# Performance work log

Measured on AMD Instinct MI355X. Metric: run time of the kernel, lower is better.

The kernel has to match this reference:

```python
import jax, jax.numpy as jnp
import numpy as np
from jax import lax

NUM_VARS = 16384
NUM_CHECKS = 8192
BATCH = 32
MAX_ITER = 15
H_DENSITY = 0.001  # ~8 ones per column, LDPC-like Tanner graph


def setup_inputs() -> dict:
    key = jax.random.key(0)
    k_h, k_s, k_l = jax.random.split(key, 3)
    # Sparse binary parity-check matrix represented densely (same math).
    parity_matrix = (jax.random.uniform(k_h, (NUM_CHECKS, NUM_VARS)) < H_DENSITY).astype(jnp.float32)
    syndrome = jax.random.randint(k_s, (BATCH, NUM_CHECKS), 0, 2).astype(jnp.float32)
    channel_llrs = jax.random.normal(k_l, (BATCH, NUM_VARS), dtype=jnp.float32)
    w_vc = jnp.ones((1,), dtype=jnp.float32)
    w_cv = jnp.ones((1,), dtype=jnp.float32)
    damping = jnp.float32(0.5)
    return {
        "syndrome": syndrome,
        "parity_matrix": parity_matrix,
        "channel_llrs": channel_llrs,
        "w_vc": w_vc,
        "w_cv": w_cv,
        "damping": damping,
    }


def reference(syndrome, parity_matrix, channel_llrs, w_vc, w_cv, damping):
    # syndrome: (B, C); parity_matrix H: (C, V); channel_llrs: (B, V)
    s_sign = 1.0 - 2.0 * syndrome  # (B, C)

    def body(v_beliefs, _):
        # v -> c: sparse.mm(H, v^T)^T == v @ H^T  -> (B, C)
        v_to_c = w_vc * (v_beliefs @ parity_matrix.T)
        c_msg = s_sign * jnp.tanh(v_to_c * 0.5)  # (B, C)
        # c -> v: sparse.mm(H^T, c^T)^T == c @ H  -> (B, V)
        c_to_v = w_cv * (c_msg @ parity_matrix)
        v_new = damping * v_beliefs + (1.0 - damping) * (channel_llrs + c_to_v)
        return v_new, None

    v_beliefs, _ = lax.scan(body, channel_llrs, None, length=MAX_ITER)
    return jax.nn.sigmoid(-v_beliefs)  # (B, V) bit-flip probabilities
```

## Files before the change

### kernel.cpp

```cpp
#include <hip/hip_runtime.h>


#define C_NUM 8192
#define V_NUM 16384
#define B_NUM 32
#define RW 64
#define CW 32

#define RQ 12
#define CQ 8

#define NBLK 256
#define NTHR 1024
#define NTH (NBLK * NTHR)

#define WCAP 256

typedef unsigned short u16;
typedef unsigned int u32;
typedef unsigned long long u64;

#define ZERO_WORDS ((C_NUM * 4 + V_NUM * 4 + C_NUM * RW * 2 + V_NUM * CW * 2) / 4)
#define NBAR 31
#define BAR_STRIDE 64

__device__ __forceinline__ float agent_ldf(const float* p) {
    return __hip_atomic_load(p, __ATOMIC_RELAXED, __HIP_MEMORY_SCOPE_AGENT);
}
__device__ __forceinline__ void agent_stf(float* p, float v) {
    __hip_atomic_store(p, v, __ATOMIC_RELAXED, __HIP_MEMORY_SCOPE_AGENT);
}
__device__ __forceinline__ u64 agent_ld64(const u64* p) {
    return __hip_atomic_load(p, __ATOMIC_RELAXED, __HIP_MEMORY_SCOPE_AGENT);
}
__device__ __forceinline__ int agent_ldi(const int* p) {
    return __hip_atomic_load(p, __ATOMIC_RELAXED, __HIP_MEMORY_SCOPE_AGENT);
}
__device__ __forceinline__ void agent_st32(u32* p, u32 v) {
    __hip_atomic_store(p, v, __ATOMIC_RELAXED, __HIP_MEMORY_SCOPE_AGENT);
}
__device__ __forceinline__ void agent_st16(u16* p, u16 v) {
    __hip_atomic_store(p, v, __ATOMIC_RELAXED, __HIP_MEMORY_SCOPE_AGENT);
}

__device__ __forceinline__ void grid_barrier(u32* bars, int id) {
    __syncthreads();
    if (threadIdx.x == 0) {
        u32* base = bars + id * 8 * BAR_STRIDE;
        asm volatile("s_waitcnt vmcnt(0) lgkmcnt(0)" ::: "memory");
        __hip_atomic_fetch_add(base + (blockIdx.x & 7) * BAR_STRIDE, 1u,
                               __ATOMIC_RELAXED, __HIP_MEMORY_SCOPE_AGENT);
        u32 sum;
        do {
            sum = 0;
#pragma unroll
            for (int g = 0; g < 8; ++g)
                sum += __hip_atomic_load(base + g * BAR_STRIDE,
                                         __ATOMIC_RELAXED, __HIP_MEMORY_SCOPE_AGENT);
            if (sum < (u32)NBLK) __builtin_amdgcn_s_sleep(4);
        } while (sum < (u32)NBLK);
        asm volatile("" ::: "memory");
    }
    __syncthreads();
}

__device__ __forceinline__ float fast_tanh_half(float x) {
    float ax = fabsf(x);
    float e = __expf(-ax);
    return copysignf((1.0f - e) / (1.0f + e), x);
}

__global__ __launch_bounds__(NTHR, 1)
void bp_fused(const float* __restrict__ H,
              const float* __restrict__ synd,
              const float* __restrict__ llr,
              const float* __restrict__ w_vc_p,
              const float* __restrict__ w_cv_p,
              const float* __restrict__ damp_p,
              int* __restrict__ row_cnt, int* __restrict__ col_cnt,
              u16* __restrict__ row_idx, u16* __restrict__ col_idx,
              float* __restrict__ bel, float* __restrict__ cms,
              u32* __restrict__ bars,
              float* __restrict__ out) {
    const int tid = blockIdx.x * NTHR + threadIdx.x;
    const int lane = threadIdx.x & 63;

    __shared__ u32 lds_edges[(NTHR / 64) * WCAP];
    __shared__ u64 ls_row64[32 * RQ];
    __shared__ u64 ls_col64[64 * CQ];
    u32* const wl = lds_edges + (threadIdx.x >> 6) * WCAP;

    {
        u32* zp = (u32*)row_cnt;
        for (int t = tid; t < ZERO_WORDS; t += NTH) agent_st32(&zp[t], 0u);
        if (tid < 32) agent_stf(&bel[V_NUM * B_NUM + tid], 0.0f);
        else if (tid < 64) agent_stf(&cms[C_NUM * B_NUM + (tid - 32)], 0.0f);
    }
    float llr_r[2], bel_r[2];
#pragma unroll
    for (int r = 0; r < 2; ++r) {
        int i = tid + r * NTH;
        int b = i & 31, v = i >> 5;
        float x = llr[b * V_NUM + v];
        llr_r[r] = x; bel_r[r] = x;
        agent_stf(&bel[i], x);
    }
    float ss_r;
    {
        int b = tid & 31, c = tid >> 5;
        ss_r = 1.0f - 2.0f * synd[b * C_NUM + c];
    }

    int wave_cnt;
    {
        const float4* Hv = (const float4*)H;
        const u64 ltmask = (1ull << lane) - 1ull;
        int wb = 0;
        int t = tid;
        float4 c0 = Hv[t];
        float4 c1 = Hv[t + NTH];
#pragma unroll 1
        for (int itn = 0; itn < 64; ++itn) {
            float4 n0, n1;
            int tn = t + 2 * NTH;
            if (itn < 63) { n0 = Hv[tn]; n1 = Hv[tn + NTH]; }
            float vals[8] = {c0.x, c0.y, c0.z, c0.w, c1.x, c1.y, c1.z, c1.w};
#pragma unroll
            for (int k = 0; k < 8; ++k) {
                bool nz = vals[k] != 0.0f;
                u64 b = __ballot(nz);
                if (b) {
                    if (nz) {
                        int ee = (k < 4) ? (t * 4 + k)
                                         : ((t + NTH) * 4 + (k - 4));
                        int off = wb + (int)__popcll(b & ltmask);
                        if (off < WCAP) wl[off] = (u32)ee;
                    }
                    wb += (int)__popcll(b);
                }
            }
            c0 = n0; c1 = n1; t = tn;
        }
        wave_cnt = wb < WCAP ? wb : WCAP;
    }
    grid_barrier(bars, 0);

    {
        for (int e = lane; e < wave_cnt; e += 64) {
            u32 ee = wl[e];
            int c = (int)(ee >> 14);
            int v = (int)(ee & (V_NUM - 1));
            int rs = atomicAdd(&row_cnt[c], 1);
            if (rs < RW) agent_st16(&row_idx[c * RW + rs], (u16)v);
            int cs = atomicAdd(&col_cnt[v], 1);
            if (cs < CW) agent_st16(&col_idx[v * CW + cs], (u16)c);
        }
    }
    grid_barrier(bars, 1);

    {
        int t = threadIdx.x;
        if (t < 32 * RQ) {
            int g = t / RQ, p = t - g * RQ;
            int c = (blockIdx.x << 5) + g;
            int n = agent_ldi(&row_cnt[c]);
            n = n > 4 * RQ ? 4 * RQ : n;
            u64 q = agent_ld64(&((const u64*)(row_idx + c * RW))[p]);
            int j = 4 * p;
            u64 a0 = (j + 0 < n) ? (q & 0xFFFFu) : (u64)V_NUM;
            u64 a1 = (j + 1 < n) ? ((q >> 16) & 0xFFFFu) : (u64)V_NUM;
            u64 a2 = (j + 2 < n) ? ((q >> 32) & 0xFFFFu) : (u64)V_NUM;
            u64 a3 = (j + 3 < n) ? (q >> 48) : (u64)V_NUM;
            ls_row64[t] = a0 | (a1 << 16) | (a2 << 32) | (a3 << 48);
        } else if (t >= 512) {
            int t2 = t - 512;
            int g = t2 >> 3, p = t2 & 7;
            int v = (g < 32) ? ((blockIdx.x << 5) + g)
                             : (C_NUM + (blockIdx.x << 5) + (g - 32));
            int n = agent_ldi(&col_cnt[v]);
            n = n > 4 * CQ ? 4 * CQ : n;
            u64 q = agent_ld64(&((const u64*)(col_idx + v * CW))[p]);
            int j = 4 * p;
            u64 a0 = (j + 0 < n) ? (q & 0xFFFFu) : (u64)C_NUM;
            u64 a1 = (j + 1 < n) ? ((q >> 16) & 0xFFFFu) : (u64)C_NUM;
            u64 a2 = (j + 2 < n) ? ((q >> 32) & 0xFFFFu) : (u64)C_NUM;
            u64 a3 = (j + 3 < n) ? (q >> 48) : (u64)C_NUM;
            ls_col64[t2] = a0 | (a1 << 16) | (a2 << 32) | (a3 << 48);
        }
    }
    int nrow_r;
    {
        int n = agent_ldi(&row_cnt[tid >> 5]);
        nrow_r = n > 4 * RQ ? 4 * RQ : n;
    }
    int ncol_r[2];
#pragma unroll
    for (int r = 0; r < 2; ++r) {
        int n = agent_ldi(&col_cnt[(tid + r * NTH) >> 5]);
        ncol_r[r] = n > 4 * CQ ? 4 * CQ : n;
    }
    const float wvc = w_vc_p[0];
    const float wcv = w_cv_p[0];
    const float d   = damp_p[0];
    __syncthreads();

    const int b_lo = tid & 31;
    const u64* const rowL  = ls_row64 + (threadIdx.x >> 5) * RQ;
    const u64* const colL0 = ls_col64 + (threadIdx.x >> 5) * CQ;
    const u64* const colL1 = ls_col64 + (32 + (threadIdx.x >> 5)) * CQ;
    int barid = 2;
    for (int it = 0; it < 15; ++it) {
        {
            float sum = 0.0f;
#pragma unroll
            for (int p = 0; p < RQ; ++p) {
                if (4 * p < nrow_r) {
                    u64 q = rowL[p];
                    int i0 = (int)(q & 0xFFFFu);
                    int i1 = (int)((q >> 16) & 0xFFFFu);
                    int i2 = (int)((q >> 32) & 0xFFFFu);
                    int i3 = (int)(q >> 48);
                    float s0 = agent_ldf(&bel[i0 * B_NUM + b_lo]);
                    float s1 = agent_ldf(&bel[i1 * B_NUM + b_lo]);
                    float s2 = agent_ldf(&bel[i2 * B_NUM + b_lo]);
                    float s3 = agent_ldf(&bel[i3 * B_NUM + b_lo]);
                    sum += s0; sum += s1; sum += s2; sum += s3;
                }
            }
            agent_stf(&cms[tid], ss_r * fast_tanh_half(wvc * sum));
        }
        grid_barrier(bars, barid++);

        bool last = (it == 14);
#pragma unroll
        for (int r = 0; r < 2; ++r) {
            const u64* colL = r ? colL1 : colL0;
            float sum = 0.0f;
#pragma unroll
            for (int p = 0; p < CQ; ++p) {
                if (4 * p < ncol_r[r]) {
                    u64 q = colL[p];
                    int i0 = (int)(q & 0xFFFFu);
                    int i1 = (int)((q >> 16) & 0xFFFFu);
                    int i2 = (int)((q >> 32) & 0xFFFFu);
                    int i3 = (int)(q >> 48);
                    float s0 = agent_ldf(&cms[i0 * B_NUM + b_lo]);
                    float s1 = agent_ldf(&cms[i1 * B_NUM + b_lo]);
                    float s2 = agent_ldf(&cms[i2 * B_NUM + b_lo]);
                    float s3 = agent_ldf(&cms[i3 * B_NUM + b_lo]);
                    sum += s0; sum += s1; sum += s2; sum += s3;
                }
            }
            float nb = d * bel_r[r] + (1.0f - d) * (llr_r[r] + wcv * sum);
            bel_r[r] = nb;
            int i = tid + r * NTH;
            if (!last) {
                agent_stf(&bel[i], nb);
            } else {
                int b = i & 31, v = i >> 5;
                out[b * V_NUM + v] = 1.0f / (1.0f + __expf(nb));
            }
        }
        if (!last) grid_barrier(bars, barid++);
    }
}

extern "C" void kernel_launch(void* const* d_in, const int* in_sizes, int n_in,
                              void* d_out, int out_size, void* d_ws, size_t ws_size,
                              hipStream_t stream) {
    const float* synd = (const float*)d_in[0];
    const float* H    = (const float*)d_in[1];
    const float* llr  = (const float*)d_in[2];
    const float* w_vc = (const float*)d_in[3];
    const float* w_cv = (const float*)d_in[4];
    const float* damp = (const float*)d_in[5];
    float* out = (float*)d_out;

    char* ws = (char*)d_ws;
    size_t off = 0;
    int* row_cnt = (int*)(ws + off); off += (size_t)C_NUM * 4;
    int* col_cnt = (int*)(ws + off); off += (size_t)V_NUM * 4;
    u16* row_idx = (u16*)(ws + off); off += (size_t)C_NUM * RW * 2;
    u16* col_idx = (u16*)(ws + off); off += (size_t)V_NUM * CW * 2;
    float* bel = (float*)(ws + off); off += (size_t)V_NUM * B_NUM * 4 + 256;
    float* cms = (float*)(ws + off); off += (size_t)C_NUM * B_NUM * 4 + 256;
    u32* bars  = (u32*)(ws + off); off += (size_t)NBAR * 8 * BAR_STRIDE * 4;

    hipMemsetAsync(bars, 0, (size_t)NBAR * 8 * BAR_STRIDE * 4, stream);

    void* args[] = {
        (void*)&H, (void*)&synd, (void*)&llr,
        (void*)&w_vc, (void*)&w_cv, (void*)&damp,
        (void*)&row_cnt, (void*)&col_cnt, (void*)&row_idx, (void*)&col_idx,
        (void*)&bel, (void*)&cms, (void*)&bars, (void*)&out
    };
    hipLaunchCooperativeKernel((const void*)bp_fused,
                               dim3(NBLK), dim3(NTHR), args, 0, stream);
}
```

Measured before the change: 927.3 us.

## Replace check-to-variable grid barrier with per-value epoch-tagged flags

Check messages are now stored as 64-bit words that pack the float with an iteration tag. They go into double-buffered arrays, and variable nodes spin on each needed message until its tag matches the current iteration. This removes one grid-wide barrier per iteration so variable updates can start as soon as their inputs are ready. The H scan prefetch is also deepened to two stages ahead. In exchange, message traffic doubles in width, extra zeroing is needed, and polling loops may add memory contention.

```diff
diff --git a/kernel.cpp b/kernel.cpp
--- a/kernel.cpp
+++ b/kernel.cpp
@@ -20,7 +20,9 @@
 typedef unsigned int u32;
 typedef unsigned long long u64;
 
-#define ZERO_WORDS ((C_NUM * 4 + V_NUM * 4 + C_NUM * RW * 2 + V_NUM * CW * 2) / 4)
+#define CSTRIDE (C_NUM * B_NUM + 32)
+#define ZW_A ((C_NUM * 4 + V_NUM * 4 + C_NUM * RW * 2 + V_NUM * CW * 2 + C_NUM * B_NUM * 8) / 4)
+#define ZW_B (C_NUM * B_NUM * 8 / 4)
 #define NBAR 31
 #define BAR_STRIDE 64
 
@@ -32,6 +34,9 @@
 }
 __device__ __forceinline__ u64 agent_ld64(const u64* p) {
     return __hip_atomic_load(p, __ATOMIC_RELAXED, __HIP_MEMORY_SCOPE_AGENT);
+}
+__device__ __forceinline__ void agent_st64(u64* p, u64 v) {
+    __hip_atomic_store(p, v, __ATOMIC_RELAXED, __HIP_MEMORY_SCOPE_AGENT);
 }
 __device__ __forceinline__ int agent_ldi(const int* p) {
     return __hip_atomic_load(p, __ATOMIC_RELAXED, __HIP_MEMORY_SCOPE_AGENT);
@@ -79,7 +84,8 @@
               const float* __restrict__ damp_p,
               int* __restrict__ row_cnt, int* __restrict__ col_cnt,
               u16* __restrict__ row_idx, u16* __restrict__ col_idx,
-              float* __restrict__ bel, float* __restrict__ cms,
+              u64* __restrict__ cmst,
+              float* __restrict__ bel,
               u32* __restrict__ bars,
               float* __restrict__ out) {
     const int tid = blockIdx.x * NTHR + threadIdx.x;
@@ -92,9 +98,14 @@
 
     {
         u32* zp = (u32*)row_cnt;
-        for (int t = tid; t < ZERO_WORDS; t += NTH) agent_st32(&zp[t], 0u);
+        for (int t = tid; t < ZW_A; t += NTH) agent_st32(&zp[t], 0u);
+        u32* zq = (u32*)(cmst + CSTRIDE);
+        for (int t = tid; t < ZW_B; t += NTH) agent_st32(&zq[t], 0u);
         if (tid < 32) agent_stf(&bel[V_NUM * B_NUM + tid], 0.0f);
-        else if (tid < 64) agent_stf(&cms[C_NUM * B_NUM + (tid - 32)], 0.0f);
+        else if (tid < 64)
+            agent_st64(&cmst[C_NUM * B_NUM + (tid - 32)], 0xFFFFFFFF00000000ull);
+        else if (tid < 96)
+            agent_st64(&cmst[CSTRIDE + C_NUM * B_NUM + (tid - 64)], 0xFFFFFFFF00000000ull);
     }
     float llr_r[2], bel_r[2];
 #pragma unroll
@@ -116,30 +127,31 @@
         const float4* Hv = (const float4*)H;
         const u64 ltmask = (1ull << lane) - 1ull;
         int wb = 0;
-        int t = tid;
-        float4 c0 = Hv[t];
-        float4 c1 = Hv[t + NTH];
+        int ta = tid;
+        int tb = tid + 2 * NTH;
+        float4 a0 = Hv[ta], a1 = Hv[ta + NTH];
+        float4 b0 = Hv[tb], b1 = Hv[tb + NTH];
 #pragma unroll 1
         for (int itn = 0; itn < 64; ++itn) {
-            float4 n0, n1;
-            int tn = t + 2 * NTH;
-            if (itn < 63) { n0 = Hv[tn]; n1 = Hv[tn + NTH]; }
-            float vals[8] = {c0.x, c0.y, c0.z, c0.w, c1.x, c1.y, c1.z, c1.w};
+            int tc = tb + 2 * NTH;
+            float4 p0, p1;
+            if (itn < 62) { p0 = Hv[tc]; p1 = Hv[tc + NTH]; }
+            float vals[8] = {a0.x, a0.y, a0.z, a0.w, a1.x, a1.y, a1.z, a1.w};
 #pragma unroll
             for (int k = 0; k < 8; ++k) {
                 bool nz = vals[k] != 0.0f;
                 u64 b = __ballot(nz);
                 if (b) {
                     if (nz) {
-                        int ee = (k < 4) ? (t * 4 + k)
-                                         : ((t + NTH) * 4 + (k - 4));
+                        int ee = (k < 4) ? (ta * 4 + k)
+                                         : ((ta + NTH) * 4 + (k - 4));
                         int off = wb + (int)__popcll(b & ltmask);
                         if (off < WCAP) wl[off] = (u32)ee;
                     }
                     wb += (int)__popcll(b);
                 }
             }
-            c0 = n0; c1 = n1; t = tn;
+            a0 = b0; a1 = b1; b0 = p0; b1 = p1; ta = tb; tb = tc;
         }
         wave_cnt = wb < WCAP ? wb : WCAP;
     }
@@ -210,6 +222,8 @@
     const u64* const colL1 = ls_col64 + (32 + (threadIdx.x >> 5)) * CQ;
     int barid = 2;
     for (int it = 0; it < 15; ++it) {
+        const u32 want = (u32)(it + 1);
+        u64* const cw = cmst + (size_t)(it & 1) * CSTRIDE;
         {
             float sum = 0.0f;
 #pragma unroll
@@ -227,9 +241,9 @@
                     sum += s0; sum += s1; sum += s2; sum += s3;
                 }
             }
-            agent_stf(&cms[tid], ss_r * fast_tanh_half(wvc * sum));
-        }
-        grid_barrier(bars, barid++);
+            float m = ss_r * fast_tanh_half(wvc * sum);
+            agent_st64(&cw[tid], ((u64)want << 32) | (u64)__float_as_uint(m));
+        }
 
         bool last = (it == 14);
 #pragma unroll
@@ -244,11 +258,30 @@
                     int i1 = (int)((q >> 16) & 0xFFFFu);
                     int i2 = (int)((q >> 32) & 0xFFFFu);
                     int i3 = (int)(q >> 48);
-                    float s0 = agent_ldf(&cms[i0 * B_NUM + b_lo]);
-                    float s1 = agent_ldf(&cms[i1 * B_NUM + b_lo]);
-                    float s2 = agent_ldf(&cms[i2 * B_NUM + b_lo]);
-                    float s3 = agent_ldf(&cms[i3 * B_NUM + b_lo]);
-                    sum += s0; sum += s1; sum += s2; sum += s3;
+                    u64* a0 = &cw[(size_t)i0 * B_NUM + b_lo];
+                    u64* a1 = &cw[(size_t)i1 * B_NUM + b_lo];
+                    u64* a2 = &cw[(size_t)i2 * B_NUM + b_lo];
+                    u64* a3 = &cw[(size_t)i3 * B_NUM + b_lo];
+                    u64 g0 = agent_ld64(a0);
+                    u64 g1 = agent_ld64(a1);
+                    u64 g2 = agent_ld64(a2);
+                    u64 g3 = agent_ld64(a3);
+                    for (;;) {
+                        bool bad0 = (u32)(g0 >> 32) < want;
+                        bool bad1 = (u32)(g1 >> 32) < want;
+                        bool bad2 = (u32)(g2 >> 32) < want;
+                        bool bad3 = (u32)(g3 >> 32) < want;
+                        if (!(bad0 | bad1 | bad2 | bad3)) break;
+                        __builtin_amdgcn_s_sleep(1);
+                        if (bad0) g0 = agent_ld64(a0);
+                        if (bad1) g1 = agent_ld64(a1);
+                        if (bad2) g2 = agent_ld64(a2);
+                        if (bad3) g3 = agent_ld64(a3);
+                    }
+                    sum += __uint_as_float((u32)g0);
+                    sum += __uint_as_float((u32)g1);
+                    sum += __uint_as_float((u32)g2);
+                    sum += __uint_as_float((u32)g3);
                 }
             }
             float nb = d * bel_r[r] + (1.0f - d) * (llr_r[r] + wcv * sum);
@@ -282,8 +315,8 @@
     int* col_cnt = (int*)(ws + off); off += (size_t)V_NUM * 4;
     u16* row_idx = (u16*)(ws + off); off += (size_t)C_NUM * RW * 2;
     u16* col_idx = (u16*)(ws + off); off += (size_t)V_NUM * CW * 2;
-    float* bel = (float*)(ws + off); off += (size_t)V_NUM * B_NUM * 4 + 256;
-    float* cms = (float*)(ws + off); off += (size_t)C_NUM * B_NUM * 4 + 256;
+    u64* cmst = (u64*)(ws + off); off += (size_t)2 * CSTRIDE * 8;
+    float* bel = (float*)(ws + off); off += (size_t)(V_NUM * B_NUM + 64) * 4;
     u32* bars  = (u32*)(ws + off); off += (size_t)NBAR * 8 * BAR_STRIDE * 4;
 
     hipMemsetAsync(bars, 0, (size_t)NBAR * 8 * BAR_STRIDE * 4, stream);
@@ -292,7 +325,7 @@
         (void*)&H, (void*)&synd, (void*)&llr,
         (void*)&w_vc, (void*)&w_cv, (void*)&damp,
         (void*)&row_cnt, (void*)&col_cnt, (void*)&row_idx, (void*)&col_idx,
-        (void*)&bel, (void*)&cms, (void*)&bars, (void*)&out
+        (void*)&cmst, (void*)&bel, (void*)&bars, (void*)&out
     };
     hipLaunchCooperativeKernel((const void*)bp_fused,
                                dim3(NBLK), dim3(NTHR), args, 0, stream);
```

Measured after the change: 925.5 us. Within noise of the previous version (-0.2%).

## Partition batch across XCDs so BP iterations use XCD-local L2 loads

Applied to the files above, without the earlier changes.

Each block reads its XCC_ID from a hardware register and takes a rank within that XCD. When all 8 XCDs hold 32 blocks each, every XCD owns 4 batch columns and stores them in its own belief and check-message slice. The iteration gathers then use sc0 loads (cached in the XCD's L2) rather than agent-scope coherent loads, which is meant to cut cross-die coherence traffic. In exchange it needs a bigger LDS footprint, drops the zeroing of row_idx and col_idx, and deepens the prefetch in the H scan. If the XCD mapping is unbalanced it falls back to agent-scope loads.

```diff
diff --git a/kernel.cpp b/kernel.cpp
--- a/kernel.cpp
+++ b/kernel.cpp
@@ -9,6 +9,8 @@
 
 #define RQ 12
 #define CQ 8
+#define RQ_S 13
+#define CQ_S 9
 
 #define NBLK 256
 #define NTHR 1024
@@ -16,12 +18,15 @@
 
 #define WCAP 256
 
+#define BEL_SL (16400 * 4)
+#define CMS_SL (8200 * 4)
+
 typedef unsigned short u16;
 typedef unsigned int u32;
 typedef unsigned long long u64;
 
-#define ZERO_WORDS ((C_NUM * 4 + V_NUM * 4 + C_NUM * RW * 2 + V_NUM * CW * 2) / 4)
-#define NBAR 31
+#define ZERO_WORDS ((C_NUM + V_NUM))
+#define NBAR 32
 #define BAR_STRIDE 64
 
 __device__ __forceinline__ float agent_ldf(const float* p) {
@@ -70,6 +75,159 @@
     return copysignf((1.0f - e) / (1.0f + e), x);
 }
 
+template<bool LOCAL>
+__device__ __forceinline__ void ld4(const float* p0, const float* p1,
+                                    const float* p2, const float* p3,
+                                    float& r0, float& r1, float& r2, float& r3) {
+    if (LOCAL) {
+        asm volatile(
+            "global_load_dword %0, %4, off sc0\n\t"
+            "global_load_dword %1, %5, off sc0\n\t"
+            "global_load_dword %2, %6, off sc0\n\t"
+            "global_load_dword %3, %7, off sc0\n\t"
+            "s_waitcnt vmcnt(0)"
+            : "=&v"(r0), "=&v"(r1), "=&v"(r2), "=&v"(r3)
+            : "v"(p0), "v"(p1), "v"(p2), "v"(p3)
+            : "memory");
+    } else {
+        r0 = agent_ldf(p0); r1 = agent_ldf(p1);
+        r2 = agent_ldf(p2); r3 = agent_ldf(p3);
+    }
+}
+
+template<bool LOCAL>
+__device__ __forceinline__ void decode_tail(
+    int G, int R,
+    const float* __restrict__ synd, const float* __restrict__ llr,
+    const int* __restrict__ row_cnt, const int* __restrict__ col_cnt,
+    const u16* __restrict__ row_idx, const u16* __restrict__ col_idx,
+    float* __restrict__ bel_x, float* __restrict__ cms_x,
+    u32* __restrict__ bars, float* __restrict__ out,
+    u64* ls_row, u64* ls_col,
+    float wvc, float wcv, float d)
+{
+    const int t = threadIdx.x;
+    const int b4 = t & 3;
+    const int qid = t >> 2;
+    float* const belS = bel_x + (size_t)G * BEL_SL;
+    float* const cmsS = cms_x + (size_t)G * CMS_SL;
+
+    for (int e = t; e < 256 * RQ; e += NTHR) {
+        int rl = e / RQ, p = e - rl * RQ;
+        int c = (R << 8) + rl;
+        int n = agent_ldi(&row_cnt[c]); n = n > 4 * RQ ? 4 * RQ : n;
+        u64 q = agent_ld64(&((const u64*)(row_idx + (size_t)c * RW))[p]);
+        int j = 4 * p;
+        u64 a0 = (j + 0 < n) ? (q & 0xFFFFu) : (u64)V_NUM;
+        u64 a1 = (j + 1 < n) ? ((q >> 16) & 0xFFFFu) : (u64)V_NUM;
+        u64 a2 = (j + 2 < n) ? ((q >> 32) & 0xFFFFu) : (u64)V_NUM;
+        u64 a3 = (j + 3 < n) ? (q >> 48) : (u64)V_NUM;
+        ls_row[rl * RQ_S + p] = a0 | (a1 << 16) | (a2 << 32) | (a3 << 48);
+    }
+    for (int e = t; e < 512 * CQ; e += NTHR) {
+        int gl = e >> 3, p = e & 7;
+        int v = (gl < 256) ? ((R << 8) + gl) : (C_NUM + (R << 8) + (gl - 256));
+        int n = agent_ldi(&col_cnt[v]); n = n > 4 * CQ ? 4 * CQ : n;
+        u64 q = agent_ld64(&((const u64*)(col_idx + (size_t)v * CW))[p]);
+        int j = 4 * p;
+        u64 a0 = (j + 0 < n) ? (q & 0xFFFFu) : (u64)C_NUM;
+        u64 a1 = (j + 1 < n) ? ((q >> 16) & 0xFFFFu) : (u64)C_NUM;
+        u64 a2 = (j + 2 < n) ? ((q >> 32) & 0xFFFFu) : (u64)C_NUM;
+        u64 a3 = (j + 3 < n) ? (q >> 48) : (u64)C_NUM;
+        ls_col[gl * CQ_S + p] = a0 | (a1 << 16) | (a2 << 32) | (a3 << 48);
+    }
+    const int c_my = (R << 8) + qid;
+    const int v0_my = (R << 8) + qid;
+    const int v1_my = C_NUM + (R << 8) + qid;
+    int nrow;  { int n = agent_ldi(&row_cnt[c_my]);  nrow  = n > 4*RQ ? 4*RQ : n; }
+    int ncol0; { int n = agent_ldi(&col_cnt[v0_my]); ncol0 = n > 4*CQ ? 4*CQ : n; }
+    int ncol1; { int n = agent_ldi(&col_cnt[v1_my]); ncol1 = n > 4*CQ ? 4*CQ : n; }
+    const int b = (G << 2) + b4;
+    const float ss = 1.0f - 2.0f * synd[b * C_NUM + c_my];
+    const float llr0 = llr[b * V_NUM + v0_my];
+    const float llr1 = llr[b * V_NUM + v1_my];
+    float bel0 = llr0, bel1 = llr1;
+    if (LOCAL) {
+        belS[v0_my * 4 + b4] = bel0;
+        belS[v1_my * 4 + b4] = bel1;
+    } else {
+        agent_stf(&belS[v0_my * 4 + b4], bel0);
+        agent_stf(&belS[v1_my * 4 + b4], bel1);
+    }
+
+    grid_barrier(bars, 2);
+
+    const u64* const rowL  = ls_row + qid * RQ_S;
+    const u64* const colL0 = ls_col + qid * CQ_S;
+    const u64* const colL1 = ls_col + (256 + qid) * CQ_S;
+    float* const cms_own  = cmsS + c_my * 4 + b4;
+    float* const bel_own0 = belS + v0_my * 4 + b4;
+    float* const bel_own1 = belS + v1_my * 4 + b4;
+
+    int barid = 3;
+    for (int it = 0; it < 15; ++it) {
+        {
+            float sum = 0.0f;
+#pragma unroll
+            for (int p = 0; p < RQ; ++p) {
+                if (4 * p < nrow) {
+                    u64 q = rowL[p];
+                    const float* a0 = belS + (int)(q & 0xFFFFu) * 4 + b4;
+                    const float* a1 = belS + (int)((q >> 16) & 0xFFFFu) * 4 + b4;
+                    const float* a2 = belS + (int)((q >> 32) & 0xFFFFu) * 4 + b4;
+                    const float* a3 = belS + (int)(q >> 48) * 4 + b4;
+                    float s0, s1, s2, s3;
+                    ld4<LOCAL>(a0, a1, a2, a3, s0, s1, s2, s3);
+                    sum += s0; sum += s1; sum += s2; sum += s3;
+                }
+            }
+            float m = ss * fast_tanh_half(wvc * sum);
+            if (LOCAL) *cms_own = m; else agent_stf(cms_own, m);
+        }
+        grid_barrier(bars, barid++);
+
+        bool last = (it == 14);
+        float sum0 = 0.0f, sum1 = 0.0f;
+#pragma unroll
+        for (int p = 0; p < CQ; ++p) {
+            if (4 * p < ncol0) {
+                u64 q = colL0[p];
+                const float* a0 = cmsS + (int)(q & 0xFFFFu) * 4 + b4;
+                const float* a1 = cmsS + (int)((q >> 16) & 0xFFFFu) * 4 + b4;
+                const float* a2 = cmsS + (int)((q >> 32) & 0xFFFFu) * 4 + b4;
+                const float* a3 = cmsS + (int)(q >> 48) * 4 + b4;
+                float s0, s1, s2, s3;
+                ld4<LOCAL>(a0, a1, a2, a3, s0, s1, s2, s3);
+                sum0 += s0; sum0 += s1; sum0 += s2; sum0 += s3;
+            }
+        }
+#pragma unroll
+        for (int p = 0; p < CQ; ++p) {
+            if (4 * p < ncol1) {
+                u64 q = colL1[p];
+                const float* a0 = cmsS + (int)(q & 0xFFFFu) * 4 + b4;
+                const float* a1 = cmsS + (int)((q >> 16) & 0xFFFFu) * 4 + b4;
+                const float* a2 = cmsS + (int)((q >> 32) & 0xFFFFu) * 4 + b4;
+                const float* a3 = cmsS + (int)(q >> 48) * 4 + b4;
+                float s0, s1, s2, s3;
+                ld4<LOCAL>(a0, a1, a2, a3, s0, s1, s2, s3);
+                sum1 += s0; sum1 += s1; sum1 += s2; sum1 += s3;
+            }
+        }
+        float nb0 = d * bel0 + (1.0f - d) * (llr0 + wcv * sum0);
+        float nb1 = d * bel1 + (1.0f - d) * (llr1 + wcv * sum1);
+        bel0 = nb0; bel1 = nb1;
+        if (!last) {
+            if (LOCAL) { *bel_own0 = nb0; *bel_own1 = nb1; }
+            else { agent_stf(bel_own0, nb0); agent_stf(bel_own1, nb1); }
+            grid_barrier(bars, barid++);
+        } else {
+            out[b * V_NUM + v0_my] = 1.0f / (1.0f + __expf(nb0));
+            out[b * V_NUM + v1_my] = 1.0f / (1.0f + __expf(nb1));
+        }
+    }
+}
+
 __global__ __launch_bounds__(NTHR, 1)
 void bp_fused(const float* __restrict__ H,
               const float* __restrict__ synd,
@@ -79,36 +237,36 @@
               const float* __restrict__ damp_p,
               int* __restrict__ row_cnt, int* __restrict__ col_cnt,
               u16* __restrict__ row_idx, u16* __restrict__ col_idx,
-              float* __restrict__ bel, float* __restrict__ cms,
-              u32* __restrict__ bars,
+              float* __restrict__ bel_x, float* __restrict__ cms_x,
+              u32* __restrict__ bars, int* __restrict__ xcd_cnt,
               float* __restrict__ out) {
     const int tid = blockIdx.x * NTHR + threadIdx.x;
     const int lane = threadIdx.x & 63;
 
-    __shared__ u32 lds_edges[(NTHR / 64) * WCAP];
-    __shared__ u64 ls_row64[32 * RQ];
-    __shared__ u64 ls_col64[64 * CQ];
+    __shared__ u32 lds_edges[(NTHR / 64) * WCAP + 1024];
+    __shared__ u64 ls_row[256 * RQ_S];
+    __shared__ u64 ls_col[512 * CQ_S];
+    __shared__ int s_xcd, s_rank;
     u32* const wl = lds_edges + (threadIdx.x >> 6) * WCAP;
+
+    if (threadIdx.x == 0) {
+        u32 x;
+        asm volatile("s_getreg_b32 %0, hwreg(HW_REG_XCC_ID)" : "=s"(x));
+        x &= 15;
+        s_xcd = (int)x;
+        s_rank = atomicAdd(&xcd_cnt[x], 1);
+    }
 
     {
         u32* zp = (u32*)row_cnt;
         for (int t = tid; t < ZERO_WORDS; t += NTH) agent_st32(&zp[t], 0u);
-        if (tid < 32) agent_stf(&bel[V_NUM * B_NUM + tid], 0.0f);
-        else if (tid < 64) agent_stf(&cms[C_NUM * B_NUM + (tid - 32)], 0.0f);
-    }
-    float llr_r[2], bel_r[2];
-#pragma unroll
-    for (int r = 0; r < 2; ++r) {
-        int i = tid + r * NTH;
-        int b = i & 31, v = i >> 5;
-        float x = llr[b * V_NUM + v];
-        llr_r[r] = x; bel_r[r] = x;
-        agent_stf(&bel[i], x);
-    }
-    float ss_r;
-    {
-        int b = tid & 31, c = tid >> 5;
-        ss_r = 1.0f - 2.0f * synd[b * C_NUM + c];
+        if (tid < 32) {
+            int g = tid >> 2, j = tid & 3;
+            agent_stf(&bel_x[(size_t)g * BEL_SL + V_NUM * 4 + j], 0.0f);
+        } else if (tid < 64) {
+            int g = (tid - 32) >> 2, j = tid & 3;
+            agent_stf(&cms_x[(size_t)g * CMS_SL + C_NUM * 4 + j], 0.0f);
+        }
     }
 
     int wave_cnt;
@@ -116,30 +274,31 @@
         const float4* Hv = (const float4*)H;
         const u64 ltmask = (1ull << lane) - 1ull;
         int wb = 0;
-        int t = tid;
-        float4 c0 = Hv[t];
-        float4 c1 = Hv[t + NTH];
+        int ta = tid;
+        int tb = tid + 2 * NTH;
+        float4 a0 = Hv[ta], a1 = Hv[ta + NTH];
+        float4 b0 = Hv[tb], b1 = Hv[tb + NTH];
 #pragma unroll 1
         for (int itn = 0; itn < 64; ++itn) {
-            float4 n0, n1;
-            int tn = t + 2 * NTH;
-            if (itn < 63) { n0 = Hv[tn]; n1 = Hv[tn + NTH]; }
-            float vals[8] = {c0.x, c0.y, c0.z, c0.w, c1.x, c1.y, c1.z, c1.w};
+            int tc = tb + 2 * NTH;
+            float4 p0, p1;
+            if (itn < 62) { p0 = Hv[tc]; p1 = Hv[tc + NTH]; }
+            float vals[8] = {a0.x, a0.y, a0.z, a0.w, a1.x, a1.y, a1.z, a1.w};
 #pragma unroll
             for (int k = 0; k < 8; ++k) {
                 bool nz = vals[k] != 0.0f;
-                u64 b = __ballot(nz);
-                if (b) {
+                u64 bb = __ballot(nz);
+                if (bb) {
                     if (nz) {
-                        int ee = (k < 4) ? (t * 4 + k)
-                                         : ((t + NTH) * 4 + (k - 4));
-                        int off = wb + (int)__popcll(b & ltmask);
+                        int ee = (k < 4) ? (ta * 4 + k)
+                                         : ((ta + NTH) * 4 + (k - 4));
+                        int off = wb + (int)__popcll(bb & ltmask);
                         if (off < WCAP) wl[off] = (u32)ee;
                     }
-                    wb += (int)__popcll(b);
+                    wb += (int)__popcll(bb);
                 }
             }
-            c0 = n0; c1 = n1; t = tn;
+            a0 = b0; a1 = b1; b0 = p0; b1 = p1; ta = tb; tb = tc;
         }
         wave_cnt = wb < WCAP ? wb : WCAP;
     }
@@ -151,117 +310,31 @@
             int c = (int)(ee >> 14);
             int v = (int)(ee & (V_NUM - 1));
             int rs = atomicAdd(&row_cnt[c], 1);
-            if (rs < RW) agent_st16(&row_idx[c * RW + rs], (u16)v);
+            if (rs < RW) agent_st16(&row_idx[(size_t)c * RW + rs], (u16)v);
             int cs = atomicAdd(&col_cnt[v], 1);
-            if (cs < CW) agent_st16(&col_idx[v * CW + cs], (u16)c);
+            if (cs < CW) agent_st16(&col_idx[(size_t)v * CW + cs], (u16)c);
         }
     }
     grid_barrier(bars, 1);
 
-    {
-        int t = threadIdx.x;
-        if (t < 32 * RQ) {
-            int g = t / RQ, p = t - g * RQ;
-            int c = (blockIdx.x << 5) + g;
-            int n = agent_ldi(&row_cnt[c]);
-            n = n > 4 * RQ ? 4 * RQ : n;
-            u64 q = agent_ld64(&((const u64*)(row_idx + c * RW))[p]);
-            int j = 4 * p;
-            u64 a0 = (j + 0 < n) ? (q & 0xFFFFu) : (u64)V_NUM;
-            u64 a1 = (j + 1 < n) ? ((q >> 16) & 0xFFFFu) : (u64)V_NUM;
-            u64 a2 = (j + 2 < n) ? ((q >> 32) & 0xFFFFu) : (u64)V_NUM;
-            u64 a3 = (j + 3 < n) ? (q >> 48) : (u64)V_NUM;
-            ls_row64[t] = a0 | (a1 << 16) | (a2 << 32) | (a3 << 48);
-        } else if (t >= 512) {
-            int t2 = t - 512;
-            int g = t2 >> 3, p = t2 & 7;
-            int v = (g < 32) ? ((blockIdx.x << 5) + g)
-                             : (C_NUM + (blockIdx.x << 5) + (g - 32));
-            int n = agent_ldi(&col_cnt[v]);
-            n = n > 4 * CQ ? 4 * CQ : n;
-            u64 q = agent_ld64(&((const u64*)(col_idx + v * CW))[p]);
-            int j = 4 * p;
-            u64 a0 = (j + 0 < n) ? (q & 0xFFFFu) : (u64)C_NUM;
-            u64 a1 = (j + 1 < n) ? ((q >> 16) & 0xFFFFu) : (u64)C_NUM;
-            u64 a2 = (j + 2 < n) ? ((q >> 32) & 0xFFFFu) : (u64)C_NUM;
-            u64 a3 = (j + 3 < n) ? (q >> 48) : (u64)C_NUM;
-            ls_col64[t2] = a0 | (a1 << 16) | (a2 << 32) | (a3 << 48);
-        }
-    }
-    int nrow_r;
-    {
-        int n = agent_ldi(&row_cnt[tid >> 5]);
-        nrow_r = n > 4 * RQ ? 4 * RQ : n;
-    }
-    int ncol_r[2];
-#pragma unroll
-    for (int r = 0; r < 2; ++r) {
-        int n = agent_ldi(&col_cnt[(tid + r * NTH) >> 5]);
-        ncol_r[r] = n > 4 * CQ ? 4 * CQ : n;
-    }
+    int my_xcd = s_xcd, my_rank = s_rank;
+    bool balanced = true;
+#pragma unroll
+    for (int g = 0; g < 8; ++g) balanced &= (agent_ldi(&xcd_cnt[g]) == 32);
+
     const float wvc = w_vc_p[0];
     const float wcv = w_cv_p[0];
     const float d   = damp_p[0];
-    __syncthreads();
-
-    const int b_lo = tid & 31;
-    const u64* const rowL  = ls_row64 + (threadIdx.x >> 5) * RQ;
-    const u64* const colL0 = ls_col64 + (threadIdx.x >> 5) * CQ;
-    const u64* const colL1 = ls_col64 + (32 + (threadIdx.x >> 5)) * CQ;
-    int barid = 2;
-    for (int it = 0; it < 15; ++it) {
-        {
-            float sum = 0.0f;
-#pragma unroll
-            for (int p = 0; p < RQ; ++p) {
-                if (4 * p < nrow_r) {
-                    u64 q = rowL[p];
-                    int i0 = (int)(q & 0xFFFFu);
-                    int i1 = (int)((q >> 16) & 0xFFFFu);
-                    int i2 = (int)((q >> 32) & 0xFFFFu);
-                    int i3 = (int)(q >> 48);
-                    float s0 = agent_ldf(&bel[i0 * B_NUM + b_lo]);
-                    float s1 = agent_ldf(&bel[i1 * B_NUM + b_lo]);
-                    float s2 = agent_ldf(&bel[i2 * B_NUM + b_lo]);
-                    float s3 = agent_ldf(&bel[i3 * B_NUM + b_lo]);
-                    sum += s0; sum += s1; sum += s2; sum += s3;
-                }
-            }
-            agent_stf(&cms[tid], ss_r * fast_tanh_half(wvc * sum));
-        }
-        grid_barrier(bars, barid++);
-
-        bool last = (it == 14);
-#pragma unroll
-        for (int r = 0; r < 2; ++r) {
-            const u64* colL = r ? colL1 : colL0;
-            float sum = 0.0f;
-#pragma unroll
-            for (int p = 0; p < CQ; ++p) {
-                if (4 * p < ncol_r[r]) {
-                    u64 q = colL[p];
-                    int i0 = (int)(q & 0xFFFFu);
-                    int i1 = (int)((q >> 16) & 0xFFFFu);
-                    int i2 = (int)((q >> 32) & 0xFFFFu);
-                    int i3 = (int)(q >> 48);
-                    float s0 = agent_ldf(&cms[i0 * B_NUM + b_lo]);
-                    float s1 = agent_ldf(&cms[i1 * B_NUM + b_lo]);
-                    float s2 = agent_ldf(&cms[i2 * B_NUM + b_lo]);
-                    float s3 = agent_ldf(&cms[i3 * B_NUM + b_lo]);
-                    sum += s0; sum += s1; sum += s2; sum += s3;
-                }
-            }
-            float nb = d * bel_r[r] + (1.0f - d) * (llr_r[r] + wcv * sum);
-            bel_r[r] = nb;
-            int i = tid + r * NTH;
-            if (!last) {
-                agent_stf(&bel[i], nb);
-            } else {
-                int b = i & 31, v = i >> 5;
-                out[b * V_NUM + v] = 1.0f / (1.0f + __expf(nb));
-            }
-        }
-        if (!last) grid_barrier(bars, barid++);
+
+    if (balanced) {
+        decode_tail<true>(my_xcd, my_rank, synd, llr, row_cnt, col_cnt,
+                          row_idx, col_idx, bel_x, cms_x, bars, out,
+                          ls_row, ls_col, wvc, wcv, d);
+    } else {
+        decode_tail<false>((int)(blockIdx.x >> 5), (int)(blockIdx.x & 31),
+                           synd, llr, row_cnt, col_cnt,
+                           row_idx, col_idx, bel_x, cms_x, bars, out,
+                           ls_row, ls_col, wvc, wcv, d);
     }
 }
 
@@ -282,17 +355,19 @@
     int* col_cnt = (int*)(ws + off); off += (size_t)V_NUM * 4;
     u16* row_idx = (u16*)(ws + off); off += (size_t)C_NUM * RW * 2;
     u16* col_idx = (u16*)(ws + off); off += (size_t)V_NUM * CW * 2;
-    float* bel = (float*)(ws + off); off += (size_t)V_NUM * B_NUM * 4 + 256;
-    float* cms = (float*)(ws + off); off += (size_t)C_NUM * B_NUM * 4 + 256;
+    float* bel_x = (float*)(ws + off); off += (size_t)8 * BEL_SL * 4;
+    float* cms_x = (float*)(ws + off); off += (size_t)8 * CMS_SL * 4;
     u32* bars  = (u32*)(ws + off); off += (size_t)NBAR * 8 * BAR_STRIDE * 4;
-
-    hipMemsetAsync(bars, 0, (size_t)NBAR * 8 * BAR_STRIDE * 4, stream);
+    int* xcd_cnt = (int*)(ws + off); off += 64;
+
+    hipMemsetAsync(bars, 0, (size_t)NBAR * 8 * BAR_STRIDE * 4 + 64, stream);
 
     void* args[] = {
         (void*)&H, (void*)&synd, (void*)&llr,
         (void*)&w_vc, (void*)&w_cv, (void*)&damp,
         (void*)&row_cnt, (void*)&col_cnt, (void*)&row_idx, (void*)&col_idx,
-        (void*)&bel, (void*)&cms, (void*)&bars, (void*)&out
+        (void*)&bel_x, (void*)&cms_x, (void*)&bars, (void*)&xcd_cnt,
+        (void*)&out
     };
     hipLaunchCooperativeKernel((const void*)bp_fused,
                                dim3(NBLK), dim3(NTHR), args, 0, stream);
```

New measurement: 921.5 us. No clear change (-0.6%).
